# Optimization experiments

Hardware: AMD Instinct MI355X
Metric: run time of the kernel (lower is better)

## Reference

```python
import jax, jax.numpy as jnp
import numpy as np

INPUT_SIZE = 8
HIDDEN = 128
BATCH = 256
SEQ = 2048


def setup_inputs() -> dict:
    key = jax.random.key(0)
    ks = jax.random.split(key, 7)
    s_ih = 1.0 / np.sqrt(HIDDEN)
    x = jax.random.normal(ks[0], (BATCH, SEQ, INPUT_SIZE), dtype=jnp.float32)
    h = jnp.zeros((1, BATCH, HIDDEN), dtype=jnp.float32)
    # nn.RNN params (uniform(-1/sqrt(hidden), 1/sqrt(hidden)) like torch init)
    W_ih = jax.random.uniform(ks[1], (HIDDEN, INPUT_SIZE), jnp.float32, -s_ih, s_ih)
    W_hh = jax.random.uniform(ks[2], (HIDDEN, HIDDEN), jnp.float32, -s_ih, s_ih)
    b_ih = jax.random.uniform(ks[3], (HIDDEN,), jnp.float32, -s_ih, s_ih)
    b_hh = jax.random.uniform(ks[4], (HIDDEN,), jnp.float32, -s_ih, s_ih)
    # temp_head: Linear(hidden, 1)
    W_head = jax.random.uniform(ks[5], (1, HIDDEN), jnp.float32, -s_ih, s_ih)
    b_head = jax.random.uniform(ks[6], (1,), jnp.float32, -s_ih, s_ih)
    return {"x": x, "h": h, "W_ih": W_ih, "W_hh": W_hh, "b_ih": b_ih,
            "b_hh": b_hh, "W_head": W_head, "b_head": b_head}


def reference(x, h, W_ih, W_hh, b_ih, b_hh, W_head, b_head):
    # x: (B, T, I), h: (1, B, H)
    # Precompute input projections for all timesteps in one GEMM: (T, B, H)
    x_proj = jnp.einsum('bti,hi->tbh', x, W_ih) + (b_ih + b_hh)

    def step(h_t, xp_t):
        h_new = jnp.tanh(xp_t + h_t @ W_hh.T)  # (B, H)
        return h_new, h_new

    h0 = h[0]  # (B, H)
    h_last, out = jax.lax.scan(step, h0, x_proj)  # out: (T, B, H)
    last_step_features = out[-1]                   # (B, H)
    pred = last_step_features @ W_head.T + b_head  # (B, 1)
    h_n = h_last[None, :, :]                       # (1, B, H)
    return (pred, last_step_features, h_n)
```

## Files before the change

kernel.cpp:

```cpp
#include <hip/hip_runtime.h>


typedef float f32x2 __attribute__((ext_vector_type(2)));
typedef float f32x4 __attribute__((ext_vector_type(4)));

#define BB 256
#define TT 2048
#define II 8
#define HH 128
#define THREADS 256

#define PK_FMA_LO(acc, hp, wp) \
    asm("v_pk_fma_f32 %0, %1, %2, %0 op_sel:[0,0,0] op_sel_hi:[0,1,1]" \
        : "+v"(acc) : "v"(hp), "v"(wp))
#define PK_FMA_HI(acc, hp, wp) \
    asm("v_pk_fma_f32 %0, %1, %2, %0 op_sel:[1,0,0] op_sel_hi:[1,1,1]" \
        : "+v"(acc) : "v"(hp), "v"(wp))

__device__ __forceinline__ float quad_sum(float x) {
    int xi = __builtin_bit_cast(int, x);
    int y1 = __builtin_amdgcn_update_dpp(0, xi, 0xB1, 0xF, 0xF, true);
    float s1 = x + __builtin_bit_cast(float, y1);
    int s1i = __builtin_bit_cast(int, s1);
    int y2 = __builtin_amdgcn_update_dpp(0, s1i, 0x4E, 0xF, 0xF, true);
    return s1 + __builtin_bit_cast(float, y2);
}

__global__ void
__launch_bounds__(THREADS, 1)
__attribute__((amdgpu_waves_per_eu(1, 1)))
rnn_v12_kernel(const float* __restrict__ x,
               const float* __restrict__ h0,
               const float* __restrict__ W_ih,
               const float* __restrict__ W_hh,
               const float* __restrict__ b_ih,
               const float* __restrict__ b_hh,
               const float* __restrict__ W_head,
               const float* __restrict__ b_head,
               float* __restrict__ out)
{
    __shared__ __align__(16) float W_lds[HH * HH];
    __shared__ __align__(16) float h_lds[2][HH];
    __shared__ float part[HH];

    const int b    = blockIdx.x;
    const int tid  = threadIdx.x;
    const int w    = tid >> 6;
    const int lane = tid & 63;
    const int jg   = lane >> 2;
    const int kc   = lane & 3;
    const int j0   = w * 32 + jg * 2;

    {
        const f32x4* Wg = (const f32x4*)W_hh;
        f32x4*       Wl = (f32x4*)W_lds;
        #pragma unroll
        for (int q = 0; q < 16; ++q)
            Wl[q * THREADS + tid] = Wg[q * THREADS + tid];
    }
    if (tid < HH) h_lds[0][tid] = h0[b * HH + tid];
    __syncthreads();

    f32x2 wj[32];
    {
        const float* r0 = W_lds + j0 * HH + kc * 32;
        const float* r1 = r0 + HH;
        #pragma unroll
        for (int i = 0; i < 8; ++i) {
            const int m = (i + 2 * kc) & 7;
            #pragma unroll
            for (int c = 0; c < 4; ++c)
                wj[4 * i + c] = (f32x2){r0[4 * m + c], r1[4 * m + c]};
        }
    }
    f32x2 wx0 = (f32x2){W_ih[j0 * II + 2 * kc],     W_ih[(j0 + 1) * II + 2 * kc]};
    f32x2 wx1 = (f32x2){W_ih[j0 * II + 2 * kc + 1], W_ih[(j0 + 1) * II + 2 * kc + 1]};
    f32x2 bias2 = (f32x2){0.25f * (b_ih[j0] + b_hh[j0]),
                          0.25f * (b_ih[j0 + 1] + b_hh[j0 + 1])};

    const float* xk = x + (size_t)b * TT * II + 2 * kc;
    f32x2 xe = *(const f32x2*)(xk + 0 * II);
    f32x2 xo = *(const f32x2*)(xk + 1 * II);

    #define STEP(XV, RBUF, TN)                                                   \
    {                                                                            \
        f32x2 a0 = bias2;                                                        \
        f32x2 a1 = (f32x2){0.f, 0.f};                                            \
        f32x2 a2 = (f32x2){0.f, 0.f};                                            \
        f32x2 a3 = (f32x2){0.f, 0.f};                                            \
        PK_FMA_LO(a0, XV, wx0);               \
        PK_FMA_HI(a1, XV, wx1);               \
        _Pragma("unroll")                                                        \
        for (int i = 0; i < 8; i += 2) {                                         \
            const f32x4 hva = *(const f32x4*)                                    \
                &h_lds[RBUF][kc * 32 + (((i + 0) + 2 * kc) & 7) * 4];            \
            const f32x4 hvb = *(const f32x4*)                                    \
                &h_lds[RBUF][kc * 32 + (((i + 1) + 2 * kc) & 7) * 4];            \
            const f32x2 ha01 = __builtin_shufflevector(hva, hva, 0, 1);          \
            const f32x2 ha23 = __builtin_shufflevector(hva, hva, 2, 3);          \
            const f32x2 hb01 = __builtin_shufflevector(hvb, hvb, 0, 1);          \
            const f32x2 hb23 = __builtin_shufflevector(hvb, hvb, 2, 3);          \
            PK_FMA_LO(a0, ha01, wj[4 * i + 0]);                                  \
            PK_FMA_HI(a1, ha01, wj[4 * i + 1]);                                  \
            PK_FMA_LO(a2, ha23, wj[4 * i + 2]);                                  \
            PK_FMA_HI(a3, ha23, wj[4 * i + 3]);                                  \
            PK_FMA_LO(a0, hb01, wj[4 * i + 4]);                                  \
            PK_FMA_HI(a1, hb01, wj[4 * i + 5]);                                  \
            PK_FMA_LO(a2, hb23, wj[4 * i + 6]);                                  \
            PK_FMA_HI(a3, hb23, wj[4 * i + 7]);                                  \
        }                                                                        \
        const f32x2 s2 = (a0 + a1) + (a2 + a3);             \
        const float s0 = quad_sum(s2.x);                                         \
        const float s1 = quad_sum(s2.y);                                         \
        const float e0 = __builtin_amdgcn_exp2f(s0 * 2.8853900817779268f);       \
        const float e1 = __builtin_amdgcn_exp2f(s1 * 2.8853900817779268f);       \
        f32x2 hn;                                                                \
        hn.x = 1.0f - 2.0f * __builtin_amdgcn_rcpf(e0 + 1.0f);                   \
        hn.y = 1.0f - 2.0f * __builtin_amdgcn_rcpf(e1 + 1.0f);                   \
        if (kc == 0) *(f32x2*)&h_lds[(RBUF) ^ 1][j0] = hn;                       \
        { const int tn_ = (TN) < TT ? (TN) : (TT - 1);                           \
          XV = *(const f32x2*)(xk + (size_t)tn_ * II); }                         \
        asm volatile("s_waitcnt lgkmcnt(0)\n\ts_barrier" ::: "memory");          \
    }

    for (int t = 0; t < TT; t += 2) {
        STEP(xe, 0, t + 2)
        STEP(xo, 1, t + 3)
    }
    #undef STEP

    if (tid < HH) {
        const float hl = h_lds[0][tid];
        out[BB + b * HH + tid]           = hl;
        out[BB + BB * HH + b * HH + tid] = hl;
        part[tid] = hl * W_head[tid];
    }
    __syncthreads();
    if (w == 0) {
        float s = part[lane] + part[lane + 64];
        #pragma unroll
        for (int off = 32; off > 0; off >>= 1) s += __shfl_down(s, off);
        if (lane == 0) out[b] = s + b_head[0];
    }
}

extern "C" void kernel_launch(void* const* d_in, const int* in_sizes, int n_in,
                              void* d_out, int out_size, void* d_ws, size_t ws_size,
                              hipStream_t stream) {
    const float* x      = (const float*)d_in[0];
    const float* h0     = (const float*)d_in[1];
    const float* W_ih   = (const float*)d_in[2];
    const float* W_hh   = (const float*)d_in[3];
    const float* b_ih   = (const float*)d_in[4];
    const float* b_hh   = (const float*)d_in[5];
    const float* W_head = (const float*)d_in[6];
    const float* b_head = (const float*)d_in[7];
    float* out = (float*)d_out;

    hipLaunchKernelGGL(rnn_v12_kernel, dim3(BB), dim3(THREADS), 0, stream,
                       x, h0, W_ih, W_hh, b_ih, b_hh, W_head, b_head, out);
}
```

Before: 602.1 us.

## Halve block threads so each lane computes four hidden units per step

Measured after the change: 853.8 us. +41.8%, slower.

```diff
diff --git a/kernel.cpp b/kernel.cpp
--- a/kernel.cpp
+++ b/kernel.cpp
@@ -8,7 +8,7 @@
 #define TT 2048
 #define II 8
 #define HH 128
-#define THREADS 256
+#define THREADS 128
 
 #define PK_FMA_LO(acc, hp, wp) \
     asm("v_pk_fma_f32 %0, %1, %2, %0 op_sel:[0,0,0] op_sel_hi:[0,1,1]" \
@@ -29,7 +29,7 @@
 __global__ void
 __launch_bounds__(THREADS, 1)
 __attribute__((amdgpu_waves_per_eu(1, 1)))
-rnn_v12_kernel(const float* __restrict__ x,
+rnn_v15_kernel(const float* __restrict__ x,
                const float* __restrict__ h0,
                const float* __restrict__ W_ih,
                const float* __restrict__ W_hh,
@@ -49,34 +49,42 @@
     const int lane = tid & 63;
     const int jg   = lane >> 2;
     const int kc   = lane & 3;
-    const int j0   = w * 32 + jg * 2;
+    const int j0   = w * 64 + jg * 4;
 
     {
         const f32x4* Wg = (const f32x4*)W_hh;
         f32x4*       Wl = (f32x4*)W_lds;
         #pragma unroll
-        for (int q = 0; q < 16; ++q)
+        for (int q = 0; q < 32; ++q)
             Wl[q * THREADS + tid] = Wg[q * THREADS + tid];
     }
-    if (tid < HH) h_lds[0][tid] = h0[b * HH + tid];
+    h_lds[0][tid] = h0[b * HH + tid];
     __syncthreads();
 
-    f32x2 wj[32];
+    f32x2 wjA[32], wjB[32];
     {
         const float* r0 = W_lds + j0 * HH + kc * 32;
         const float* r1 = r0 + HH;
+        const float* r2 = r0 + 2 * HH;
+        const float* r3 = r0 + 3 * HH;
         #pragma unroll
         for (int i = 0; i < 8; ++i) {
             const int m = (i + 2 * kc) & 7;
             #pragma unroll
-            for (int c = 0; c < 4; ++c)
-                wj[4 * i + c] = (f32x2){r0[4 * m + c], r1[4 * m + c]};
+            for (int c = 0; c < 4; ++c) {
+                wjA[4 * i + c] = (f32x2){r0[4 * m + c], r1[4 * m + c]};
+                wjB[4 * i + c] = (f32x2){r2[4 * m + c], r3[4 * m + c]};
+            }
         }
     }
-    f32x2 wx0 = (f32x2){W_ih[j0 * II + 2 * kc],     W_ih[(j0 + 1) * II + 2 * kc]};
-    f32x2 wx1 = (f32x2){W_ih[j0 * II + 2 * kc + 1], W_ih[(j0 + 1) * II + 2 * kc + 1]};
-    f32x2 bias2 = (f32x2){0.25f * (b_ih[j0] + b_hh[j0]),
-                          0.25f * (b_ih[j0 + 1] + b_hh[j0 + 1])};
+    const f32x2 wx01_0 = (f32x2){W_ih[j0 * II + 2 * kc],       W_ih[(j0 + 1) * II + 2 * kc]};
+    const f32x2 wx01_1 = (f32x2){W_ih[j0 * II + 2 * kc + 1],   W_ih[(j0 + 1) * II + 2 * kc + 1]};
+    const f32x2 wx23_0 = (f32x2){W_ih[(j0 + 2) * II + 2 * kc], W_ih[(j0 + 3) * II + 2 * kc]};
+    const f32x2 wx23_1 = (f32x2){W_ih[(j0 + 2) * II + 2 * kc + 1], W_ih[(j0 + 3) * II + 2 * kc + 1]};
+    const f32x2 b01 = (f32x2){0.25f * (b_ih[j0] + b_hh[j0]),
+                              0.25f * (b_ih[j0 + 1] + b_hh[j0 + 1])};
+    const f32x2 b23 = (f32x2){0.25f * (b_ih[j0 + 2] + b_hh[j0 + 2]),
+                              0.25f * (b_ih[j0 + 3] + b_hh[j0 + 3])};
 
     const float* xk = x + (size_t)b * TT * II + 2 * kc;
     f32x2 xe = *(const f32x2*)(xk + 0 * II);
@@ -84,12 +92,14 @@
 
     #define STEP(XV, RBUF, TN)                                                   \
     {                                                                            \
-        f32x2 a0 = bias2;                                                        \
-        f32x2 a1 = (f32x2){0.f, 0.f};                                            \
-        f32x2 a2 = (f32x2){0.f, 0.f};                                            \
-        f32x2 a3 = (f32x2){0.f, 0.f};                                            \
-        PK_FMA_LO(a0, XV, wx0);               \
-        PK_FMA_HI(a1, XV, wx1);               \
+        f32x2 a0 = b01, a1 = (f32x2){0.f, 0.f};                                  \
+        f32x2 a2 = (f32x2){0.f, 0.f}, a3 = (f32x2){0.f, 0.f};                    \
+        f32x2 c0 = b23, c1 = (f32x2){0.f, 0.f};                                  \
+        f32x2 c2 = (f32x2){0.f, 0.f}, c3 = (f32x2){0.f, 0.f};                    \
+        PK_FMA_LO(a0, XV, wx01_0);                                               \
+        PK_FMA_HI(a1, XV, wx01_1);                                               \
+        PK_FMA_LO(c0, XV, wx23_0);                                               \
+        PK_FMA_HI(c1, XV, wx23_1);                                               \
         _Pragma("unroll")                                                        \
         for (int i = 0; i < 8; i += 2) {                                         \
             const f32x4 hva = *(const f32x4*)                                    \
@@ -100,24 +110,39 @@
             const f32x2 ha23 = __builtin_shufflevector(hva, hva, 2, 3);          \
             const f32x2 hb01 = __builtin_shufflevector(hvb, hvb, 0, 1);          \
             const f32x2 hb23 = __builtin_shufflevector(hvb, hvb, 2, 3);          \
-            PK_FMA_LO(a0, ha01, wj[4 * i + 0]);                                  \
-            PK_FMA_HI(a1, ha01, wj[4 * i + 1]);                                  \
-            PK_FMA_LO(a2, ha23, wj[4 * i + 2]);                                  \
-            PK_FMA_HI(a3, ha23, wj[4 * i + 3]);                                  \
-            PK_FMA_LO(a0, hb01, wj[4 * i + 4]);                                  \
-            PK_FMA_HI(a1, hb01, wj[4 * i + 5]);                                  \
-            PK_FMA_LO(a2, hb23, wj[4 * i + 6]);                                  \
-            PK_FMA_HI(a3, hb23, wj[4 * i + 7]);                                  \
+            PK_FMA_LO(a0, ha01, wjA[4 * i + 0]);                                 \
+            PK_FMA_HI(a1, ha01, wjA[4 * i + 1]);                                 \
+            PK_FMA_LO(a2, ha23, wjA[4 * i + 2]);                                 \
+            PK_FMA_HI(a3, ha23, wjA[4 * i + 3]);                                 \
+            PK_FMA_LO(c0, ha01, wjB[4 * i + 0]);                                 \
+            PK_FMA_HI(c1, ha01, wjB[4 * i + 1]);                                 \
+            PK_FMA_LO(c2, ha23, wjB[4 * i + 2]);                                 \
+            PK_FMA_HI(c3, ha23, wjB[4 * i + 3]);                                 \
+            PK_FMA_LO(a0, hb01, wjA[4 * i + 4]);                                 \
+            PK_FMA_HI(a1, hb01, wjA[4 * i + 5]);                                 \
+            PK_FMA_LO(a2, hb23, wjA[4 * i + 6]);                                 \
+            PK_FMA_HI(a3, hb23, wjA[4 * i + 7]);                                 \
+            PK_FMA_LO(c0, hb01, wjB[4 * i + 4]);                                 \
+            PK_FMA_HI(c1, hb01, wjB[4 * i + 5]);                                 \
+            PK_FMA_LO(c2, hb23, wjB[4 * i + 6]);                                 \
+            PK_FMA_HI(c3, hb23, wjB[4 * i + 7]);                                 \
         }                                                                        \
-        const f32x2 s2 = (a0 + a1) + (a2 + a3);             \
-        const float s0 = quad_sum(s2.x);                                         \
-        const float s1 = quad_sum(s2.y);                                         \
+        const f32x2 s01 = (a0 + a1) + (a2 + a3);                                 \
+        const f32x2 s23 = (c0 + c1) + (c2 + c3);                                 \
+        const float s0 = quad_sum(s01.x);                                        \
+        const float s1 = quad_sum(s01.y);                                        \
+        const float s2 = quad_sum(s23.x);                                        \
+        const float s3 = quad_sum(s23.y);                                        \
         const float e0 = __builtin_amdgcn_exp2f(s0 * 2.8853900817779268f);       \
         const float e1 = __builtin_amdgcn_exp2f(s1 * 2.8853900817779268f);       \
-        f32x2 hn;                                                                \
-        hn.x = 1.0f - 2.0f * __builtin_amdgcn_rcpf(e0 + 1.0f);                   \
-        hn.y = 1.0f - 2.0f * __builtin_amdgcn_rcpf(e1 + 1.0f);                   \
-        if (kc == 0) *(f32x2*)&h_lds[(RBUF) ^ 1][j0] = hn;                       \
+        const float e2 = __builtin_amdgcn_exp2f(s2 * 2.8853900817779268f);       \
+        const float e3 = __builtin_amdgcn_exp2f(s3 * 2.8853900817779268f);       \
+        f32x4 th;                                                                \
+        th.x = 1.0f - 2.0f * __builtin_amdgcn_rcpf(e0 + 1.0f);                   \
+        th.y = 1.0f - 2.0f * __builtin_amdgcn_rcpf(e1 + 1.0f);                   \
+        th.z = 1.0f - 2.0f * __builtin_amdgcn_rcpf(e2 + 1.0f);                   \
+        th.w = 1.0f - 2.0f * __builtin_amdgcn_rcpf(e3 + 1.0f);                   \
+        if (kc == 0) *(f32x4*)&h_lds[(RBUF) ^ 1][j0] = th;                       \
         { const int tn_ = (TN) < TT ? (TN) : (TT - 1);                           \
           XV = *(const f32x2*)(xk + (size_t)tn_ * II); }                         \
         asm volatile("s_waitcnt lgkmcnt(0)\n\ts_barrier" ::: "memory");          \
@@ -129,7 +154,7 @@
     }
     #undef STEP
 
-    if (tid < HH) {
+    {
         const float hl = h_lds[0][tid];
         out[BB + b * HH + tid]           = hl;
         out[BB + BB * HH + b * HH + tid] = hl;
@@ -157,6 +182,6 @@
     const float* b_head = (const float*)d_in[7];
     float* out = (float*)d_out;
 
-    hipLaunchKernelGGL(rnn_v12_kernel, dim3(BB), dim3(THREADS), 0, stream,
+    hipLaunchKernelGGL(rnn_v15_kernel, dim3(BB), dim3(THREADS), 0, stream,
                        x, h0, W_ih, W_hh, b_ih, b_hh, W_head, b_head, out);
 }
```
